# Optimization experiments

Measured on AMD Instinct MI355X. Metric: run time of the kernel, lower is better.

The kernel has to match this reference:

```python
import jax, jax.numpy as jnp
import numpy as np

# module hyperparameters (from init_kwargs)
R_MIN, R_MAX = 0.01, 0.6
RH, RW = 64, 64          # retinal_H, retinal_W
H, W = 64, 128           # output pooled H, W
UFR, UFT = 4, 4          # upsampling factors


def make_grid(weight):
    """Vectorized version of get_grid. weight: [B,2].
    Faithful to source: only the top-left [H, W] corner of the
    [H*UFR, W*UFT] grid is written; the rest (torch.empty in the
    original) is set to 0 here for determinism."""
    i = jnp.arange(H, dtype=jnp.float32)
    j = jnp.arange(W, dtype=jnp.float32)
    xg = (i - (H // 2)) / (H / 2.0)
    yg = (j - (W // 2)) / (W / 2.0)
    xx, yy = jnp.meshgrid(xg, yg, indexing="ij")  # [H,W]
    # clamp radius to avoid log(0) = -inf at the center pixel; the resulting
    # coordinate is far out of [-1,1] and gets border-clamped either way.
    logr = jnp.log(jnp.maximum(jnp.sqrt(xx ** 2 + yy ** 2), 1e-12))  # [H,W]
    lo = jnp.log(weight[:, 0] * R_MIN)[:, None, None]  # [B,1,1]
    hi = jnp.log(weight[:, 1] * R_MAX)[:, None, None]  # [B,1,1]
    r = RH * (logr[None] - lo) / (hi - lo)             # [B,H,W]
    a = jnp.arctan2(yy, xx)
    a = jnp.where(a > 0, a, 2.0 * np.pi + a)
    t = 0.5 * a * RW / np.pi                           # [H,W]
    gx = jnp.broadcast_to((t / (RW / 2.0) - 1.0)[None], r.shape)
    gy = r / (RH / 2.0) - 1.0
    small = jnp.stack([gx, gy], axis=-1)               # [B,H,W,2]
    grid = jnp.zeros((weight.shape[0], H * UFR, W * UFT, 2), jnp.float32)
    return grid.at[:, :H, :W, :].set(small)


def grid_sample_border(x, grid):
    """torch.F.grid_sample, mode=bilinear, padding_mode=border, align_corners=False.
    x: [B,C,Hin,Win], grid: [B,Hg,Wg,2] -> [B,C,Hg,Wg]."""
    B, C, Hin, Win = x.shape
    gx, gy = grid[..., 0], grid[..., 1]
    ix = jnp.clip(((gx + 1.0) * Win - 1.0) * 0.5, 0.0, Win - 1.0)
    iy = jnp.clip(((gy + 1.0) * Hin - 1.0) * 0.5, 0.0, Hin - 1.0)
    x0f = jnp.floor(ix)
    y0f = jnp.floor(iy)
    wx = (ix - x0f)[..., None]
    wy = (iy - y0f)[..., None]
    x0 = jnp.clip(x0f.astype(jnp.int32), 0, Win - 1)
    y0 = jnp.clip(y0f.astype(jnp.int32), 0, Hin - 1)
    x1 = jnp.clip(x0 + 1, 0, Win - 1)
    y1 = jnp.clip(y0 + 1, 0, Hin - 1)
    bidx = jnp.arange(B)[:, None, None]
    gather = lambda yi, xi: x[bidx, :, yi, xi]  # [B,Hg,Wg,C]
    out = (gather(y0, x0) * (1 - wx) * (1 - wy)
           + gather(y0, x1) * wx * (1 - wy)
           + gather(y1, x0) * (1 - wx) * wy
           + gather(y1, x1) * wx * wy)
    return jnp.transpose(out, (0, 3, 1, 2))  # [B,C,Hg,Wg]


def setup_inputs() -> dict:
    key = jax.random.key(0)
    k1, k2, k3, k4, k5, k6 = jax.random.split(key, 6)
    B, C, Hin, Win = 8, 64, 224, 224
    Cmid = C // 2  # int(channel * r)
    return {
        "x": jax.random.normal(k1, (B, C, Hin, Win), jnp.float32),
        "l_t_prev": jax.random.uniform(k2, (B, 2), jnp.float32),
        "w1": jax.random.normal(k3, (C, Cmid), jnp.float32) * 0.1,
        "b1": jnp.zeros((Cmid,), jnp.float32),
        "w2": jax.random.normal(k4, (Cmid, 2), jnp.float32) * 0.1,
        "b2": jnp.zeros((2,), jnp.float32),
    }


def reference(x, l_t_prev, w1, b1, w2, b2):
    # att: global avg pool -> fc -> sigmoid
    branch = x.mean(axis=(2, 3))                              # [B,C]
    weight = jax.nn.sigmoid(jax.nn.relu(branch @ w1 + b1) @ w2 + b2)  # [B,2]
    grid = make_grid(weight) + l_t_prev[:, None, None, :]     # [B,Hg,Wg,2]
    sampled = grid_sample_border(x, grid)                     # [B,C,Hg,Wg]
    B, C = sampled.shape[:2]
    pooled = sampled.reshape(B, C, H, UFR, W, UFT).mean(axis=(3, 5))  # AvgPool2d([UFR,UFT])
    return pooled, weight
```

## Files before the change

### kernel.cpp

```cpp
#include <hip/hip_runtime.h>
#include <math.h>

#define B 8
#define C 64
#define HIN 224
#define WIN 224
#define PLANE (HIN*WIN)
#define PLANE4 (PLANE/4)
#define QUART (PLANE4/4)
#define OH 64
#define OW 128
#define OUT_PER_BC (OH*OW)
#define NGRID (OH*OW)
#define POOLED_SIZE (B*C*OH*OW)

#define WS_PARTIAL 0
#define WS_COORDS 4096

#define PI_F 3.14159265358979323846f

__device__ __forceinline__ float bilinear(const float* __restrict__ p,
                                          float ix, float iy) {
    float x0f = floorf(ix), y0f = floorf(iy);
    int x0 = (int)x0f, y0 = (int)y0f;
    float wx = ix - x0f, wy = iy - y0f;
    int x1 = min(x0 + 1, WIN - 1);
    int y1 = min(y0 + 1, HIN - 1);
    const float* r0 = p + y0 * WIN;
    const float* r1 = p + y1 * WIN;
    float v00 = r0[x0], v01 = r0[x1], v10 = r1[x0], v11 = r1[x1];
    float v0 = v00 + (v01 - v00) * wx;
    float v1 = v10 + (v11 - v10) * wx;
    return v0 + (v1 - v0) * wy;
}

__global__ __launch_bounds__(256) void k1_gap_fill(const float* __restrict__ x,
                                                   const float* __restrict__ l_t,
                                                   float* __restrict__ ws,
                                                   float* __restrict__ out) {
    int blk = blockIdx.x;
    int bc  = blk >> 2, q = blk & 3;
    int b   = bc >> 6;
    int tid = threadIdx.x;

    const float4* p = (const float4*)x + (size_t)bc * PLANE4 + q * QUART;
    float s = 0.f;
#pragma unroll
    for (int k = 0; k < 12; ++k) {
        float4 v = p[tid + k * 256];
        s += (v.x + v.y) + (v.z + v.w);
    }
    if (tid < QUART - 12 * 256) {
        float4 v = p[tid + 12 * 256];
        s += (v.x + v.y) + (v.z + v.w);
    }

    const float* plane = x + (size_t)bc * PLANE;
    float gx = l_t[b * 2 + 0], gy = l_t[b * 2 + 1];
    float ixc = fminf(fmaxf(((gx + 1.f) * (float)WIN - 1.f) * 0.5f, 0.f), (float)(WIN - 1));
    float iyc = fminf(fmaxf(((gy + 1.f) * (float)HIN - 1.f) * 0.5f, 0.f), (float)(HIN - 1));
    float vc = bilinear(plane, ixc, iyc);
    float4 vc4 = make_float4(vc, vc, vc, vc);

    float4* o4 = (float4*)(out + (size_t)bc * OUT_PER_BC);
    if (q == 0) {
#pragma unroll
        for (int k = 0; k < 2; ++k) {
            int f4i = tid + k * 256;
            if (f4i < 384) {
                int row = f4i / 24;
                int c4  = f4i - row * 24 + 8;
                o4[row * 32 + c4] = vc4;
            }
        }
    } else {
        o4[q * 512 + tid]       = vc4;
        o4[q * 512 + 256 + tid] = vc4;
    }

    for (int off = 32; off; off >>= 1) s += __shfl_down(s, off, 64);
    __shared__ float lds[4];
    if ((tid & 63) == 0) lds[tid >> 6] = s;
    __syncthreads();
    if (tid == 0) ws[WS_PARTIAL + blk] = lds[0] + lds[1] + lds[2] + lds[3];
}

__global__ __launch_bounds__(256) void k2_coords(const float* __restrict__ w1,
                                                 const float* __restrict__ b1,
                                                 const float* __restrict__ w2,
                                                 const float* __restrict__ b2,
                                                 const float* __restrict__ l_t,
                                                 const float* __restrict__ ws,
                                                 float* __restrict__ out_weight,
                                                 float2* __restrict__ coords) {
    int tid = threadIdx.x;
    int blk = blockIdx.x;
    int b   = blk >> 5;

    __shared__ float branch[C];
    __shared__ float hidden[32];
    __shared__ float wpair[2];

    if (tid < C) {
        const float* pp = ws + WS_PARTIAL + (b * C + tid) * 4;
        branch[tid] = (pp[0] + pp[1] + pp[2] + pp[3]) * (1.0f / PLANE);
    }
    __syncthreads();
    if (tid < 32) {
        float h = b1[tid];
        for (int c = 0; c < C; ++c) h += branch[c] * w1[c * 32 + tid];
        hidden[tid] = h > 0.f ? h : 0.f;
    }
    __syncthreads();
    if (tid < 2) {
        float sacc = b2[tid];
        for (int m = 0; m < 32; ++m) sacc += hidden[m] * w2[m * 2 + tid];
        float wv = 1.f / (1.f + expf(-sacc));
        wpair[tid] = wv;
        if ((blk & 31) == 0) out_weight[b * 2 + tid] = wv;
    }
    __syncthreads();

    float w0  = wpair[0];
    float w1v = wpair[1];
    float lo = logf(w0 * 0.01f);
    float hi = logf(w1v * 0.6f);

    int p   = blk * 256 + tid;
    int rem = p & 8191;
    int i = rem >> 7;
    int j = rem & 127;
    float xg = (float)(i - 32) * (1.f / 32.f);
    float yg = (float)(j - 64) * (1.f / 64.f);
    float rr = sqrtf(xg * xg + yg * yg);
    float logr = logf(fmaxf(rr, 1e-12f));
    float r = 64.f * (logr - lo) / (hi - lo);
    float a = atan2f(yg, xg);
    if (!(a > 0.f)) a = 2.f * PI_F + a;
    float t = 0.5f * a * 64.f / PI_F;
    float gxv = t * (1.f / 32.f) - 1.f + l_t[b * 2 + 0];
    float gyv = r * (1.f / 32.f) - 1.f + l_t[b * 2 + 1];
    float ix = ((gxv + 1.f) * (float)WIN - 1.f) * 0.5f;
    float iy = ((gyv + 1.f) * (float)HIN - 1.f) * 0.5f;
    ix = fminf(fmaxf(ix, 0.f), (float)(WIN - 1));
    iy = fminf(fmaxf(iy, 0.f), (float)(HIN - 1));
    coords[p] = make_float2(ix, iy);
}

__global__ __launch_bounds__(256) void k3_corner(const float* __restrict__ x,
                                                 const float2* __restrict__ coords,
                                                 float* __restrict__ out) {
    int blk   = blockIdx.x;
    int bc    = blk >> 4;
    int patch = blk & 15;
    int b     = bc >> 6;
    int pb_h  = patch >> 2;
    int pb_w  = patch & 3;

    int tid    = threadIdx.x;
    int wave   = tid >> 6;
    int lane   = tid & 63;
    int wave_h = wave >> 1;
    int wave_w = wave & 1;
    int fi_l   = lane >> 3;
    int fj_l   = lane & 7;

    int fi  = pb_h * 16 + wave_h * 8 + fi_l;
    int fjb = pb_w * 32 + wave_w * 16;

    const float*  plane = x + (size_t)bc * PLANE;
    const float2* cb    = coords + b * NGRID + fi * 128 + fjb;

    float2 c0 = cb[fj_l];
    float2 c1 = cb[8 + fj_l];
    float a0 = bilinear(plane, c0.x, c0.y);
    float a1 = bilinear(plane, c1.x, c1.y);

    a0 += __shfl_xor(a0, 1, 64);  a1 += __shfl_xor(a1, 1, 64);
    a0 += __shfl_xor(a0, 2, 64);  a1 += __shfl_xor(a1, 2, 64);
    a0 += __shfl_xor(a0, 8, 64);  a1 += __shfl_xor(a1, 8, 64);
    a0 += __shfl_xor(a0, 16, 64); a1 += __shfl_xor(a1, 16, 64);

    if ((lane & 27) == 0) {
        int ph = pb_h * 4 + wave_h * 2 + (fi_l >> 2);
        int pw = pb_w * 8 + wave_w * 4 + (fj_l >> 2);
        float* o = out + (size_t)bc * OUT_PER_BC + ph * 128 + pw;
        o[0] = a0 * (1.f / 16.f);
        o[2] = a1 * (1.f / 16.f);
    }
}

extern "C" void kernel_launch(void* const* d_in, const int* in_sizes, int n_in,
                              void* d_out, int out_size, void* d_ws, size_t ws_size,
                              hipStream_t stream) {
    const float* x   = (const float*)d_in[0];
    const float* l_t = (const float*)d_in[1];
    const float* w1  = (const float*)d_in[2];
    const float* b1  = (const float*)d_in[3];
    const float* w2  = (const float*)d_in[4];
    const float* b2  = (const float*)d_in[5];
    float* out = (float*)d_out;
    float* ws  = (float*)d_ws;

    k1_gap_fill<<<dim3(B * C * 4), dim3(256), 0, stream>>>(x, l_t, ws, out);
    k2_coords<<<dim3(NGRID * B / 256), dim3(256), 0, stream>>>(
        w1, b1, w2, b2, l_t, ws, out + POOLED_SIZE, (float2*)(ws + WS_COORDS));
    k3_corner<<<dim3(B * C * 16), dim3(256), 0, stream>>>(
        x, (const float2*)(ws + WS_COORDS), out);
}
```

Baseline: 177.7 us.

## Fuse attention MLP and grid coordinate computation into the sampling kernel

Removes the separate coordinate kernel and its workspace buffer. Each sampling block now recomputes the small MLP (64x32 then 32x2) to get the per-batch log-radius bounds, and computes its own grid coordinates inline before the bilinear sampling. This drops one kernel launch and the global round trip of the coordinate array. In exchange, 8192 blocks each redo the MLP and the transcendental coordinate math, which adds serial per-block work ahead of the gathers.

```diff
diff --git a/kernel.cpp b/kernel.cpp
--- a/kernel.cpp
+++ b/kernel.cpp
@@ -11,11 +11,9 @@
 #define OH 64
 #define OW 128
 #define OUT_PER_BC (OH*OW)
-#define NGRID (OH*OW)
 #define POOLED_SIZE (B*C*OH*OW)
 
 #define WS_PARTIAL 0
-#define WS_COORDS 4096
 
 #define PI_F 3.14159265358979323846f
 
@@ -85,21 +83,24 @@
     if (tid == 0) ws[WS_PARTIAL + blk] = lds[0] + lds[1] + lds[2] + lds[3];
 }
 
-__global__ __launch_bounds__(256) void k2_coords(const float* __restrict__ w1,
-                                                 const float* __restrict__ b1,
-                                                 const float* __restrict__ w2,
-                                                 const float* __restrict__ b2,
-                                                 const float* __restrict__ l_t,
-                                                 const float* __restrict__ ws,
-                                                 float* __restrict__ out_weight,
-                                                 float2* __restrict__ coords) {
-    int tid = threadIdx.x;
-    int blk = blockIdx.x;
-    int b   = blk >> 5;
+__global__ __launch_bounds__(256) void k3_fused(const float* __restrict__ x,
+                                                const float* __restrict__ w1,
+                                                const float* __restrict__ b1,
+                                                const float* __restrict__ w2,
+                                                const float* __restrict__ b2,
+                                                const float* __restrict__ l_t,
+                                                const float* __restrict__ ws,
+                                                float* __restrict__ out_weight,
+                                                float* __restrict__ out) {
+    int blk   = blockIdx.x;
+    int bc    = blk >> 4;
+    int patch = blk & 15;
+    int b     = bc >> 6;
+    int tid   = threadIdx.x;
 
     __shared__ float branch[C];
     __shared__ float hidden[32];
-    __shared__ float wpair[2];
+    __shared__ float sparams[4];
 
     if (tid < C) {
         const float* pp = ws + WS_PARTIAL + (b * C + tid) * 4;
@@ -116,48 +117,16 @@
         float sacc = b2[tid];
         for (int m = 0; m < 32; ++m) sacc += hidden[m] * w2[m * 2 + tid];
         float wv = 1.f / (1.f + expf(-sacc));
-        wpair[tid] = wv;
-        if ((blk & 31) == 0) out_weight[b * 2 + tid] = wv;
-    }
-    __syncthreads();
-
-    float w0  = wpair[0];
-    float w1v = wpair[1];
-    float lo = logf(w0 * 0.01f);
-    float hi = logf(w1v * 0.6f);
-
-    int p   = blk * 256 + tid;
-    int rem = p & 8191;
-    int i = rem >> 7;
-    int j = rem & 127;
-    float xg = (float)(i - 32) * (1.f / 32.f);
-    float yg = (float)(j - 64) * (1.f / 64.f);
-    float rr = sqrtf(xg * xg + yg * yg);
-    float logr = logf(fmaxf(rr, 1e-12f));
-    float r = 64.f * (logr - lo) / (hi - lo);
-    float a = atan2f(yg, xg);
-    if (!(a > 0.f)) a = 2.f * PI_F + a;
-    float t = 0.5f * a * 64.f / PI_F;
-    float gxv = t * (1.f / 32.f) - 1.f + l_t[b * 2 + 0];
-    float gyv = r * (1.f / 32.f) - 1.f + l_t[b * 2 + 1];
-    float ix = ((gxv + 1.f) * (float)WIN - 1.f) * 0.5f;
-    float iy = ((gyv + 1.f) * (float)HIN - 1.f) * 0.5f;
-    ix = fminf(fmaxf(ix, 0.f), (float)(WIN - 1));
-    iy = fminf(fmaxf(iy, 0.f), (float)(HIN - 1));
-    coords[p] = make_float2(ix, iy);
-}
-
-__global__ __launch_bounds__(256) void k3_corner(const float* __restrict__ x,
-                                                 const float2* __restrict__ coords,
-                                                 float* __restrict__ out) {
-    int blk   = blockIdx.x;
-    int bc    = blk >> 4;
-    int patch = blk & 15;
-    int b     = bc >> 6;
-    int pb_h  = patch >> 2;
-    int pb_w  = patch & 3;
-
-    int tid    = threadIdx.x;
+        if ((bc & 63) == 0 && patch == 0) out_weight[b * 2 + tid] = wv;
+        sparams[tid]     = logf(wv * (tid == 0 ? 0.01f : 0.6f));
+        sparams[2 + tid] = l_t[b * 2 + tid];
+    }
+    __syncthreads();
+
+    float lo  = sparams[0], hi = sparams[1];
+    float inv_hl = 1.f / (hi - lo);
+    float ltx = sparams[2], lty = sparams[3];
+
     int wave   = tid >> 6;
     int lane   = tid & 63;
     int wave_h = wave >> 1;
@@ -165,16 +134,43 @@
     int fi_l   = lane >> 3;
     int fj_l   = lane & 7;
 
-    int fi  = pb_h * 16 + wave_h * 8 + fi_l;
-    int fjb = pb_w * 32 + wave_w * 16;
-
-    const float*  plane = x + (size_t)bc * PLANE;
-    const float2* cb    = coords + b * NGRID + fi * 128 + fjb;
-
-    float2 c0 = cb[fj_l];
-    float2 c1 = cb[8 + fj_l];
-    float a0 = bilinear(plane, c0.x, c0.y);
-    float a1 = bilinear(plane, c1.x, c1.y);
+    int pb_h = patch >> 2;
+    int pb_w = patch & 3;
+    int fi   = pb_h * 16 + wave_h * 8 + fi_l;
+    int fjb  = pb_w * 32 + wave_w * 16;
+    int fj0  = fjb + fj_l;
+    int fj1  = fjb + 8 + fj_l;
+
+    float xg = (float)(fi - 32) * (1.f / 32.f);
+    float ix0, iy0, ix1, iy1;
+    {
+        float yg = (float)(fj0 - 64) * (1.f / 64.f);
+        float rr = sqrtf(xg * xg + yg * yg);
+        float r  = 64.f * (logf(fmaxf(rr, 1e-12f)) - lo) * inv_hl;
+        float a  = atan2f(yg, xg);
+        if (!(a > 0.f)) a = 2.f * PI_F + a;
+        float t  = a * (32.f / PI_F);
+        float gxv = t * (1.f / 32.f) - 1.f + ltx;
+        float gyv = r * (1.f / 32.f) - 1.f + lty;
+        ix0 = fminf(fmaxf(((gxv + 1.f) * (float)WIN - 1.f) * 0.5f, 0.f), (float)(WIN - 1));
+        iy0 = fminf(fmaxf(((gyv + 1.f) * (float)HIN - 1.f) * 0.5f, 0.f), (float)(HIN - 1));
+    }
+    {
+        float yg = (float)(fj1 - 64) * (1.f / 64.f);
+        float rr = sqrtf(xg * xg + yg * yg);
+        float r  = 64.f * (logf(fmaxf(rr, 1e-12f)) - lo) * inv_hl;
+        float a  = atan2f(yg, xg);
+        if (!(a > 0.f)) a = 2.f * PI_F + a;
+        float t  = a * (32.f / PI_F);
+        float gxv = t * (1.f / 32.f) - 1.f + ltx;
+        float gyv = r * (1.f / 32.f) - 1.f + lty;
+        ix1 = fminf(fmaxf(((gxv + 1.f) * (float)WIN - 1.f) * 0.5f, 0.f), (float)(WIN - 1));
+        iy1 = fminf(fmaxf(((gyv + 1.f) * (float)HIN - 1.f) * 0.5f, 0.f), (float)(HIN - 1));
+    }
+
+    const float* plane = x + (size_t)bc * PLANE;
+    float a0 = bilinear(plane, ix0, iy0);
+    float a1 = bilinear(plane, ix1, iy1);
 
     a0 += __shfl_xor(a0, 1, 64);  a1 += __shfl_xor(a1, 1, 64);
     a0 += __shfl_xor(a0, 2, 64);  a1 += __shfl_xor(a1, 2, 64);
@@ -203,8 +199,6 @@
     float* ws  = (float*)d_ws;
 
     k1_gap_fill<<<dim3(B * C * 4), dim3(256), 0, stream>>>(x, l_t, ws, out);
-    k2_coords<<<dim3(NGRID * B / 256), dim3(256), 0, stream>>>(
-        w1, b1, w2, b2, l_t, ws, out + POOLED_SIZE, (float2*)(ws + WS_COORDS));
-    k3_corner<<<dim3(B * C * 16), dim3(256), 0, stream>>>(
-        x, (const float2*)(ws + WS_COORDS), out);
-}
+    k3_fused<<<dim3(B * C * 16), dim3(256), 0, stream>>>(
+        x, w1, b1, w2, b2, l_t, ws, out + POOLED_SIZE, out);
+}
```

New measurement: 185.1 us. 4.2% more time.

## Fuse three kernels into one cooperative kernel with grid syncs

Applied to the files above, without the earlier changes.

Merges the global-average-pool/fill, coordinate and corner-sampling kernels into a single cooperative launch of 1024 blocks, separated by grid-wide barriers. The reduction work is repartitioned to half-planes per block, and each block processes 8 corner units in the last phase. The aim is to remove two kernel launch gaps. In exchange it adds grid.sync costs and leaves many blocks idle during the coordinate phase, and it falls back to three separate launches if the cooperative launch fails.

```diff
diff --git a/kernel.cpp b/kernel.cpp
--- a/kernel.cpp
+++ b/kernel.cpp
@@ -1,5 +1,8 @@
 #include <hip/hip_runtime.h>
+#include <hip/hip_cooperative_groups.h>
 #include <math.h>
+
+namespace cg = cooperative_groups;
 
 #define B 8
 #define C 64
@@ -7,12 +10,12 @@
 #define WIN 224
 #define PLANE (HIN*WIN)
 #define PLANE4 (PLANE/4)
-#define QUART (PLANE4/4)
+#define HALF4 (PLANE4/2)
 #define OH 64
 #define OW 128
 #define OUT_PER_BC (OH*OW)
+#define POOLED_SIZE (B*C*OH*OW)
 #define NGRID (OH*OW)
-#define POOLED_SIZE (B*C*OH*OW)
 
 #define WS_PARTIAL 0
 #define WS_COORDS 4096
@@ -34,24 +37,24 @@
     return v0 + (v1 - v0) * wy;
 }
 
-__global__ __launch_bounds__(256) void k1_gap_fill(const float* __restrict__ x,
-                                                   const float* __restrict__ l_t,
-                                                   float* __restrict__ ws,
-                                                   float* __restrict__ out) {
-    int blk = blockIdx.x;
-    int bc  = blk >> 2, q = blk & 3;
-    int b   = bc >> 6;
-    int tid = threadIdx.x;
-
-    const float4* p = (const float4*)x + (size_t)bc * PLANE4 + q * QUART;
+__device__ __forceinline__ void phaseA(int blk, int tid,
+                                       const float* __restrict__ x,
+                                       const float* __restrict__ l_t,
+                                       float* __restrict__ ws,
+                                       float* __restrict__ out,
+                                       float* lds4) {
+    int bc = blk >> 1, half = blk & 1;
+    int b  = bc >> 6;
+
+    const float4* p = (const float4*)x + (size_t)bc * PLANE4 + half * HALF4;
     float s = 0.f;
 #pragma unroll
-    for (int k = 0; k < 12; ++k) {
+    for (int k = 0; k < 24; ++k) {
         float4 v = p[tid + k * 256];
         s += (v.x + v.y) + (v.z + v.w);
     }
-    if (tid < QUART - 12 * 256) {
-        float4 v = p[tid + 12 * 256];
+    if (tid < HALF4 - 24 * 256) {
+        float4 v = p[tid + 24 * 256];
         s += (v.x + v.y) + (v.z + v.w);
     }
 
@@ -63,47 +66,38 @@
     float4 vc4 = make_float4(vc, vc, vc, vc);
 
     float4* o4 = (float4*)(out + (size_t)bc * OUT_PER_BC);
-    if (q == 0) {
 #pragma unroll
-        for (int k = 0; k < 2; ++k) {
-            int f4i = tid + k * 256;
-            if (f4i < 384) {
-                int row = f4i / 24;
-                int c4  = f4i - row * 24 + 8;
-                o4[row * 32 + c4] = vc4;
-            }
+    for (int k = 0; k < 4; ++k) {
+        int local = tid + k * 256;
+        if (local < 960) {
+            int idx = half * 960 + local;
+            int row, col;
+            if (idx < 384) { row = idx / 24; col = 8 + (idx - row * 24); }
+            else { int t2 = idx - 384; row = 16 + (t2 >> 5); col = t2 & 31; }
+            o4[row * 32 + col] = vc4;
         }
-    } else {
-        o4[q * 512 + tid]       = vc4;
-        o4[q * 512 + 256 + tid] = vc4;
     }
 
     for (int off = 32; off; off >>= 1) s += __shfl_down(s, off, 64);
-    __shared__ float lds[4];
-    if ((tid & 63) == 0) lds[tid >> 6] = s;
-    __syncthreads();
-    if (tid == 0) ws[WS_PARTIAL + blk] = lds[0] + lds[1] + lds[2] + lds[3];
-}
-
-__global__ __launch_bounds__(256) void k2_coords(const float* __restrict__ w1,
-                                                 const float* __restrict__ b1,
-                                                 const float* __restrict__ w2,
-                                                 const float* __restrict__ b2,
-                                                 const float* __restrict__ l_t,
-                                                 const float* __restrict__ ws,
-                                                 float* __restrict__ out_weight,
-                                                 float2* __restrict__ coords) {
-    int tid = threadIdx.x;
-    int blk = blockIdx.x;
-    int b   = blk >> 5;
-
-    __shared__ float branch[C];
-    __shared__ float hidden[32];
-    __shared__ float wpair[2];
-
+    if ((tid & 63) == 0) lds4[tid >> 6] = s;
+    __syncthreads();
+    if (tid == 0) ws[WS_PARTIAL + blk] = lds4[0] + lds4[1] + lds4[2] + lds4[3];
+}
+
+__device__ __forceinline__ void phaseB(int blk, int tid,
+                                       const float* __restrict__ w1,
+                                       const float* __restrict__ b1,
+                                       const float* __restrict__ w2,
+                                       const float* __restrict__ b2,
+                                       const float* __restrict__ l_t,
+                                       const float* __restrict__ ws,
+                                       float* __restrict__ out_weight,
+                                       float2* __restrict__ coords,
+                                       float* branch, float* hidden, float* wpair) {
+    int b = blk >> 5;
     if (tid < C) {
-        const float* pp = ws + WS_PARTIAL + (b * C + tid) * 4;
-        branch[tid] = (pp[0] + pp[1] + pp[2] + pp[3]) * (1.0f / PLANE);
+        const float* pp = ws + WS_PARTIAL + (b * C + tid) * 2;
+        branch[tid] = (pp[0] + pp[1]) * (1.0f / PLANE);
     }
     __syncthreads();
     if (tid < 32) {
@@ -121,10 +115,8 @@
     }
     __syncthreads();
 
-    float w0  = wpair[0];
-    float w1v = wpair[1];
-    float lo = logf(w0 * 0.01f);
-    float hi = logf(w1v * 0.6f);
+    float lo = logf(wpair[0] * 0.01f);
+    float hi = logf(wpair[1] * 0.6f);
 
     int p   = blk * 256 + tid;
     int rem = p & 8191;
@@ -133,8 +125,7 @@
     float xg = (float)(i - 32) * (1.f / 32.f);
     float yg = (float)(j - 64) * (1.f / 64.f);
     float rr = sqrtf(xg * xg + yg * yg);
-    float logr = logf(fmaxf(rr, 1e-12f));
-    float r = 64.f * (logr - lo) / (hi - lo);
+    float r = 64.f * (logf(fmaxf(rr, 1e-12f)) - lo) / (hi - lo);
     float a = atan2f(yg, xg);
     if (!(a > 0.f)) a = 2.f * PI_F + a;
     float t = 0.5f * a * 64.f / PI_F;
@@ -147,17 +138,16 @@
     coords[p] = make_float2(ix, iy);
 }
 
-__global__ __launch_bounds__(256) void k3_corner(const float* __restrict__ x,
-                                                 const float2* __restrict__ coords,
-                                                 float* __restrict__ out) {
-    int blk   = blockIdx.x;
-    int bc    = blk >> 4;
-    int patch = blk & 15;
+__device__ __forceinline__ void phaseC_unit(int unit, int tid,
+                                            const float* __restrict__ x,
+                                            const float2* __restrict__ coords,
+                                            float* __restrict__ out) {
+    int bc    = unit >> 4;
+    int patch = unit & 15;
     int b     = bc >> 6;
     int pb_h  = patch >> 2;
     int pb_w  = patch & 3;
 
-    int tid    = threadIdx.x;
     int wave   = tid >> 6;
     int lane   = tid & 63;
     int wave_h = wave >> 1;
@@ -188,6 +178,63 @@
         o[0] = a0 * (1.f / 16.f);
         o[2] = a1 * (1.f / 16.f);
     }
+}
+
+__global__ __launch_bounds__(256, 4) void fused_all(const float* __restrict__ x,
+                                                    const float* __restrict__ l_t,
+                                                    const float* __restrict__ w1,
+                                                    const float* __restrict__ b1,
+                                                    const float* __restrict__ w2,
+                                                    const float* __restrict__ b2,
+                                                    float* __restrict__ ws,
+                                                    float* __restrict__ out) {
+    __shared__ float lds4[4];
+    __shared__ float branch[C];
+    __shared__ float hidden[32];
+    __shared__ float wpair[2];
+
+    cg::grid_group grid = cg::this_grid();
+    int blk = blockIdx.x;
+    int tid = threadIdx.x;
+
+    phaseA(blk, tid, x, l_t, ws, out, lds4);
+    grid.sync();
+    if (blk < 256)
+        phaseB(blk, tid, w1, b1, w2, b2, l_t, ws, out + POOLED_SIZE,
+               (float2*)(ws + WS_COORDS), branch, hidden, wpair);
+    grid.sync();
+#pragma unroll
+    for (int u = 0; u < 8; ++u)
+        phaseC_unit(blk * 8 + u, tid, x, (const float2*)(ws + WS_COORDS), out);
+}
+
+__global__ __launch_bounds__(256) void k1_gap_fill(const float* __restrict__ x,
+                                                   const float* __restrict__ l_t,
+                                                   float* __restrict__ ws,
+                                                   float* __restrict__ out) {
+    __shared__ float lds4[4];
+    phaseA(blockIdx.x, threadIdx.x, x, l_t, ws, out, lds4);
+}
+
+__global__ __launch_bounds__(256) void k2_coords(const float* __restrict__ w1,
+                                                 const float* __restrict__ b1,
+                                                 const float* __restrict__ w2,
+                                                 const float* __restrict__ b2,
+                                                 const float* __restrict__ l_t,
+                                                 const float* __restrict__ ws,
+                                                 float* __restrict__ out_weight,
+                                                 float2* __restrict__ coords) {
+    __shared__ float branch[C];
+    __shared__ float hidden[32];
+    __shared__ float wpair[2];
+    phaseB(blockIdx.x, threadIdx.x, w1, b1, w2, b2, l_t, ws, out_weight, coords,
+           branch, hidden, wpair);
+}
+
+__global__ __launch_bounds__(256) void k3_corner(const float* __restrict__ x,
+                                                 const float2* __restrict__ coords,
+                                                 float* __restrict__ out) {
+    phaseC_unit(blockIdx.x, threadIdx.x, x, coords, out);
 }
 
 extern "C" void kernel_launch(void* const* d_in, const int* in_sizes, int n_in,
@@ -202,9 +249,16 @@
     float* out = (float*)d_out;
     float* ws  = (float*)d_ws;
 
-    k1_gap_fill<<<dim3(B * C * 4), dim3(256), 0, stream>>>(x, l_t, ws, out);
-    k2_coords<<<dim3(NGRID * B / 256), dim3(256), 0, stream>>>(
-        w1, b1, w2, b2, l_t, ws, out + POOLED_SIZE, (float2*)(ws + WS_COORDS));
-    k3_corner<<<dim3(B * C * 16), dim3(256), 0, stream>>>(
-        x, (const float2*)(ws + WS_COORDS), out);
-}
+    void* args[] = { (void*)&x, (void*)&l_t, (void*)&w1, (void*)&b1,
+                     (void*)&w2, (void*)&b2, (void*)&ws, (void*)&out };
+    hipError_t e = hipLaunchCooperativeKernel((const void*)fused_all,
+                                              dim3(1024), dim3(256),
+                                              args, 0, stream);
+    if (e != hipSuccess) {
+        k1_gap_fill<<<dim3(1024), dim3(256), 0, stream>>>(x, l_t, ws, out);
+        k2_coords<<<dim3(256), dim3(256), 0, stream>>>(
+            w1, b1, w2, b2, l_t, ws, out + POOLED_SIZE, (float2*)(ws + WS_COORDS));
+        k3_corner<<<dim3(B * C * 16), dim3(256), 0, stream>>>(
+            x, (const float2*)(ws + WS_COORDS), out);
+    }
+}
```

New measurement: 405.9 us. +128.5%, slower.
